# Kernel optimization log

Measured on AMD Instinct MI355X. Metric: run time of the kernel, lower is better.

The kernel has to match this reference:

```python
import jax, jax.numpy as jnp
import numpy as np

ALPHA = 1.702
LIMIT = 7.0

# Tiling: A*B*M = BD*S (total dispatched tokens)
A, B, E, M, H, I = 2, 8, 16, 128, 2048, 2048
_BD, _S = 2, 1024


def setup_inputs() -> dict:
    key = jax.random.key(0)
    ks = jax.random.split(key, 6)
    inv_h = 1.0 / np.sqrt(H)
    inv_i = 1.0 / np.sqrt(I)
    return {
        "dispatched": jax.random.normal(ks[0], (A, B, E, M, H), dtype=jnp.float32),
        "gate_up_proj": jax.random.normal(ks[1], (E, H, 2 * I), dtype=jnp.float32) * inv_h,
        "gate_up_proj_bias": jax.random.normal(ks[2], (E, 2 * I), dtype=jnp.float32) * 0.02,
        "down_proj": jax.random.normal(ks[3], (E, I, H), dtype=jnp.float32) * inv_i,
        "down_proj_bias": jax.random.normal(ks[4], (E, H), dtype=jnp.float32) * 0.02,
        "sparsity_remap": jax.random.randint(ks[5], (E, E), 0, E, dtype=jnp.int32),
        "BD": _BD,
        "S": _S,
    }


def _moe_activation_gpt_oss(gate_up_out):
    # interleaved gate/up: [g0,u0,g1,u1,...]
    gate = gate_up_out[..., ::2]
    up = gate_up_out[..., 1::2]
    gate = jnp.minimum(gate, LIMIT)
    up = jnp.clip(up, -LIMIT, LIMIT)
    glu = gate * jax.nn.sigmoid(gate * ALPHA)
    return (up + 1.0) * glu


def reference(dispatched, gate_up_proj, gate_up_proj_bias, down_proj,
              down_proj_bias, sparsity_remap, BD, S):
    # sparsity_remap is an opaque tile remap for tt.sparse_matmul; the dense
    # grouped matmul computes the same math (zero tiles contribute zeros).
    a, b, e, m, h = dispatched.shape
    inter = gate_up_proj.shape[-1] // 2
    # grouped gate_up GEMM: [A,B,E,M,H] @ [E,H,2I] -> [A,B,E,M,2I]
    gate_up_out = jnp.einsum('abemh,ehn->abemn', dispatched, gate_up_proj)
    gate_up_out = gate_up_out + gate_up_proj_bias[None, None, :, None, :]
    activated = _moe_activation_gpt_oss(gate_up_out)  # [A,B,E,M,I]
    activated = activated.reshape(a * b, e, m, inter)
    # grouped down GEMM: [AB,E,M,I] @ [E,I,H] -> [AB,E,M,H]
    down_out = jnp.einsum('xemi,eih->xemh', activated, down_proj)
    down_out = down_out + down_proj_bias[None, :, None, :]
    # untile: [AB,E,M,H] -> [AB,M,E,H] -> [BD,S,E,H]
    down_out = jnp.transpose(down_out, (0, 2, 1, 3))
    return down_out.reshape(BD, S, e, h)
```

## Files before the change

kernel.cpp:

```cpp
#include <hip/hip_runtime.h>
#include <stdint.h>

#define DEV __device__ __forceinline__

constexpr int E_ = 16, M_ = 128, H_ = 2048, I_ = 2048;
constexpr int X_ = 16;
constexpr int N1 = 2 * I_;
constexpr int ROWS = X_ * M_;

typedef short bfrag __attribute__((ext_vector_type(8)));
typedef float ffrag __attribute__((ext_vector_type(4)));
typedef unsigned short us8 __attribute__((ext_vector_type(8)));

DEV unsigned short f2bf(float f) {
    union { float f; unsigned u; } v; v.f = f;
    unsigned u = v.u;
    u += 0x7fffu + ((u >> 16) & 1u);
    return (unsigned short)(u >> 16);
}

DEV void gload16(const void* g, void* lds_wave_base) {
    __builtin_amdgcn_global_load_lds(
        (const __attribute__((address_space(1))) unsigned int*)g,
        (__attribute__((address_space(3))) unsigned int*)lds_wave_base,
        16, 0, 0);
}

DEV void block_bar() {
    asm volatile("" ::: "memory");
    __builtin_amdgcn_s_barrier();
    asm volatile("" ::: "memory");
}


__global__ __launch_bounds__(256) void convert_a(const float* __restrict__ in,
                                                 unsigned short* __restrict__ outb) {
    const int n4 = X_ * E_ * M_ * H_ / 4;
    int idx = blockIdx.x * 256 + threadIdx.x;
    int stride = gridDim.x * 256;
    for (int f = idx; f < n4; f += stride) {
        float4 v = ((const float4*)in)[f];
        ushort4 o;
        o.x = f2bf(v.x); o.y = f2bf(v.y); o.z = f2bf(v.z); o.w = f2bf(v.w);
        const int c = f & 511;
        const int row = f >> 9;
        const int m = row & 127, e = (row >> 7) & 15, x = row >> 11;
        ((ushort4*)outb)[((size_t)(e * ROWS + x * M_ + m) << 9) + c] = o;
    }
}

__global__ __launch_bounds__(256) void convert_b1(const float* __restrict__ gup,
                                                  unsigned short* __restrict__ b1t) {
    const int e = blockIdx.x, h0 = blockIdx.y * 64, n0 = blockIdx.z * 128;
    __shared__ float2 tile2[64][64];
    const float* src = gup + (size_t)e * H_ * N1;
    const int t = threadIdx.x;
#pragma unroll
    for (int i = 0; i < 8; ++i) {
        int idx = i * 1024 + t * 4;
        int r = idx >> 7, c = idx & 127;
        float4 v = *(const float4*)(src + (size_t)(h0 + r) * N1 + n0 + c);
        *(float4*)&tile2[r][c >> 1] = v;
    }
    __syncthreads();
    const int p = t >> 2;
    const int hh = (t & 3) * 16;
    us8 g0, g1, u0, u1;
#pragma unroll
    for (int k = 0; k < 8; ++k) {
        float2 a = tile2[hh + k][p];
        float2 b = tile2[hh + 8 + k][p];
        g0[k] = f2bf(a.x); u0[k] = f2bf(a.y);
        g1[k] = f2bf(b.x); u1[k] = f2bf(b.y);
    }
    unsigned short* dg = b1t + ((size_t)e * N1 + (n0 >> 1) + p) * H_ + h0 + hh;
    unsigned short* du = b1t + ((size_t)e * N1 + I_ + (n0 >> 1) + p) * H_ + h0 + hh;
    *(us8*)dg = g0; *(us8*)(dg + 8) = g1;
    *(us8*)du = u0; *(us8*)(du + 8) = u1;
}

__global__ __launch_bounds__(256) void convert_b2(const float* __restrict__ dwn,
                                                  unsigned short* __restrict__ b2t) {
    const int e = blockIdx.x, i0 = blockIdx.y * 64, h0 = blockIdx.z * 64;
    __shared__ float tile[64][65];
    const float* src = dwn + (size_t)e * I_ * H_;
    const int t = threadIdx.x;
#pragma unroll
    for (int it = 0; it < 4; ++it) {
        int idx = it * 1024 + t * 4;
        int r = idx >> 6, c = idx & 63;
        float4 v = *(const float4*)(src + (size_t)(i0 + r) * H_ + h0 + c);
        tile[r][c] = v.x; tile[r][c + 1] = v.y; tile[r][c + 2] = v.z; tile[r][c + 3] = v.w;
    }
    __syncthreads();
    const int hl = t >> 2, ii = (t & 3) * 16;
    us8 o0, o1;
#pragma unroll
    for (int k = 0; k < 8; ++k) {
        o0[k] = f2bf(tile[ii + k][hl]);
        o1[k] = f2bf(tile[ii + 8 + k][hl]);
    }
    unsigned short* d = b2t + ((size_t)e * H_ + h0 + hl) * I_ + i0 + ii;
    *(us8*)d = o0; *(us8*)(d + 8) = o1;
}

template <int MODE>
__global__ __launch_bounds__(512, 2) void gemm8p(
    const unsigned short* __restrict__ A,
    const unsigned short* __restrict__ B,
    const float* __restrict__ bias,
    void* __restrict__ outv)
{
    constexpr int LD = 2048;
    constexpr int NT = 2048 / 64;

    __shared__ unsigned short lds[2][2][256 * 64];

    const int t = threadIdx.x, wave = t >> 6, lane = t & 63;
    const int wr = wave >> 2, wc = wave & 3;

    int id = blockIdx.x;
    const int cpx = gridDim.x >> 3;
    id = (id & 7) * cpx + (id >> 3);
    int e, mt, bt;
    if (MODE == 0) { e = id >> 7; mt = (id >> 4) & 7; bt = id & 15; }
    else           { e = id >> 6; mt = (id >> 3) & 7; bt = id & 7; }

    const unsigned short* Aexp = A + ((size_t)e * ROWS + mt * 256) * LD;
    const unsigned short* Bexp = (MODE == 0)
        ? B + (size_t)e * N1 * LD
        : B + ((size_t)e * H_ + bt * 256) * LD;

    ffrag acc[8][4];
#pragma unroll
    for (int i = 0; i < 8; ++i)
#pragma unroll
        for (int j = 0; j < 4; ++j) acc[i][j] = ffrag{0.f, 0.f, 0.f, 0.f};

    const int rsub = lane >> 3;
    const int csw = ((lane & 7) ^ (lane >> 3)) * 8;

    auto stage = [&](int kt, int b) {
        const int k0 = kt * 64;
#pragma unroll
        for (int i = 0; i < 4; ++i) {
            const int Rb = (wave * 4 + i) * 8;
            const int r = Rb + rsub;
            gload16(Aexp + (size_t)r * LD + k0 + csw, (void*)&lds[b][0][Rb * 64]);
        }
#pragma unroll
        for (int i = 0; i < 4; ++i) {
            const int Rb = (wave * 4 + i) * 8;
            const int r = Rb + rsub;
            int grow;
            if (MODE == 0)
                grow = ((r >> 5) & 1) * I_ + bt * 128 + (r >> 6) * 32 + (r & 31);
            else
                grow = r;
            gload16(Bexp + (size_t)grow * LD + k0 + csw, (void*)&lds[b][1][Rb * 64]);
        }
    };

    stage(0, 0);

    const int l15 = lane & 15, lr16 = lane >> 4, sw = lane & 7;
    const int arow0 = wr * 128 + l15;
    const int brow0 = wc * 64 + l15;

#pragma unroll 2
    for (int kt = 0; kt < NT; ++kt) {
        const int cur = kt & 1;

        asm volatile("s_waitcnt vmcnt(0)" ::: "memory");
        __builtin_amdgcn_sched_barrier(0);
        block_bar();

        bfrag bB0[2][2], bB1[2][2];
        bfrag af[4][2];

#pragma unroll
        for (int nf = 0; nf < 2; ++nf)
#pragma unroll
            for (int ks = 0; ks < 2; ++ks)
                bB0[nf][ks] = *(const bfrag*)&lds[cur][1][(brow0 + nf * 16) * 64 + (((ks * 4 + lr16) ^ sw) * 8)];
#pragma unroll
        for (int mf = 0; mf < 4; ++mf)
#pragma unroll
            for (int ks = 0; ks < 2; ++ks)
                af[mf][ks] = *(const bfrag*)&lds[cur][0][(arow0 + mf * 16) * 64 + (((ks * 4 + lr16) ^ sw) * 8)];
        asm volatile("" ::: "memory");
#pragma unroll
        for (int nf = 0; nf < 2; ++nf)
#pragma unroll
            for (int ks = 0; ks < 2; ++ks)
                bB1[nf][ks] = *(const bfrag*)&lds[cur][1][(brow0 + 32 + nf * 16) * 64 + (((ks * 4 + lr16) ^ sw) * 8)];

        if (kt + 1 < NT) stage(kt + 1, cur ^ 1);

        asm volatile("s_waitcnt lgkmcnt(4)" ::: "memory");
        __builtin_amdgcn_sched_barrier(0);
        __builtin_amdgcn_s_setprio(1);
#pragma unroll
        for (int mf = 0; mf < 4; ++mf)
#pragma unroll
            for (int nf = 0; nf < 2; ++nf)
#pragma unroll
                for (int ks = 0; ks < 2; ++ks)
                    acc[mf][nf] = __builtin_amdgcn_mfma_f32_16x16x32_bf16(
                        af[mf][ks], bB0[nf][ks], acc[mf][nf], 0, 0, 0);
        __builtin_amdgcn_s_setprio(0);

        asm volatile("s_waitcnt lgkmcnt(0)" ::: "memory");
        __builtin_amdgcn_sched_barrier(0);
        __builtin_amdgcn_s_setprio(1);
#pragma unroll
        for (int mf = 0; mf < 4; ++mf)
#pragma unroll
            for (int nf = 0; nf < 2; ++nf)
#pragma unroll
                for (int ks = 0; ks < 2; ++ks)
                    acc[mf][2 + nf] = __builtin_amdgcn_mfma_f32_16x16x32_bf16(
                        af[mf][ks], bB1[nf][ks], acc[mf][2 + nf], 0, 0, 0);
        __builtin_amdgcn_s_setprio(0);

        bfrag ag[4][2];
#pragma unroll
        for (int mf = 0; mf < 4; ++mf)
#pragma unroll
            for (int ks = 0; ks < 2; ++ks)
                ag[mf][ks] = *(const bfrag*)&lds[cur][0][(arow0 + 64 + mf * 16) * 64 + (((ks * 4 + lr16) ^ sw) * 8)];

        asm volatile("s_waitcnt lgkmcnt(4)" ::: "memory");
        __builtin_amdgcn_sched_barrier(0);
        __builtin_amdgcn_s_setprio(1);
#pragma unroll
        for (int mf = 0; mf < 2; ++mf)
#pragma unroll
            for (int nf = 0; nf < 2; ++nf)
#pragma unroll
                for (int ks = 0; ks < 2; ++ks)
                    acc[4 + mf][2 + nf] = __builtin_amdgcn_mfma_f32_16x16x32_bf16(
                        ag[mf][ks], bB1[nf][ks], acc[4 + mf][2 + nf], 0, 0, 0);
        __builtin_amdgcn_s_setprio(0);

        asm volatile("s_waitcnt lgkmcnt(0)" ::: "memory");
        __builtin_amdgcn_sched_barrier(0);
        __builtin_amdgcn_s_setprio(1);
#pragma unroll
        for (int mf = 2; mf < 4; ++mf)
#pragma unroll
            for (int nf = 0; nf < 2; ++nf)
#pragma unroll
                for (int ks = 0; ks < 2; ++ks)
                    acc[4 + mf][2 + nf] = __builtin_amdgcn_mfma_f32_16x16x32_bf16(
                        ag[mf][ks], bB1[nf][ks], acc[4 + mf][2 + nf], 0, 0, 0);
#pragma unroll
        for (int mf = 0; mf < 4; ++mf)
#pragma unroll
            for (int nf = 0; nf < 2; ++nf)
#pragma unroll
                for (int ks = 0; ks < 2; ++ks)
                    acc[4 + mf][nf] = __builtin_amdgcn_mfma_f32_16x16x32_bf16(
                        ag[mf][ks], bB0[nf][ks], acc[4 + mf][nf], 0, 0, 0);
        __builtin_amdgcn_s_setprio(0);
    }

    const int rb = mt * 256 + wr * 128 + lr16 * 4;
    if (MODE == 0) {
        unsigned short* act = (unsigned short*)outv + (size_t)e * ROWS * I_;
#pragma unroll
        for (int nf = 0; nf < 2; ++nf) {
            const int jj = bt * 128 + wc * 32 + nf * 16 + l15;
            const float gb = bias[(size_t)e * N1 + 2 * jj];
            const float ub = bias[(size_t)e * N1 + 2 * jj + 1];
#pragma unroll
            for (int mf = 0; mf < 8; ++mf)
#pragma unroll
                for (int r = 0; r < 4; ++r) {
                    float g = acc[mf][nf][r] + gb;
                    float u = acc[mf][2 + nf][r] + ub;
                    g = fminf(g, 7.0f);
                    u = fminf(fmaxf(u, -7.0f), 7.0f);
                    const float glu = g / (1.0f + __expf(-1.702f * g));
                    const float av = (u + 1.0f) * glu;
                    act[(size_t)(rb + mf * 16 + r) * I_ + jj] = f2bf(av);
                }
        }
    } else {
        float* out = (float*)outv;
#pragma unroll
        for (int nf = 0; nf < 4; ++nf) {
            const int h = bt * 256 + wc * 64 + nf * 16 + l15;
            const float bb = bias[(size_t)e * H_ + h];
#pragma unroll
            for (int mf = 0; mf < 8; ++mf)
#pragma unroll
                for (int r = 0; r < 4; ++r) {
                    const int row = rb + mf * 16 + r;
                    out[((size_t)row * E_ + e) * H_ + h] = acc[mf][nf][r] + bb;
                }
        }
    }
}


extern "C" void kernel_launch(void* const* d_in, const int* in_sizes, int n_in,
                              void* d_out, int out_size, void* d_ws, size_t ws_size,
                              hipStream_t stream) {
    const float* disp  = (const float*)d_in[0];
    const float* gup   = (const float*)d_in[1];
    const float* gub   = (const float*)d_in[2];
    const float* down  = (const float*)d_in[3];
    const float* dbias = (const float*)d_in[4];
    float* out = (float*)d_out;

    const size_t NEED = (size_t)512 << 20;
    if (ws_size < NEED) {
        hipMemsetAsync(d_out, 0, (size_t)out_size * sizeof(float), stream);
        return;
    }
    unsigned short* a_bf = (unsigned short*)d_ws;
    unsigned short* b1t  = (unsigned short*)((char*)d_ws + ((size_t)128 << 20));
    unsigned short* b2t  = b1t;
    unsigned short* actb = (unsigned short*)((char*)d_ws + ((size_t)384 << 20));

    convert_a<<<4096, 256, 0, stream>>>(disp, a_bf);
    convert_b1<<<dim3(E_, H_ / 64, N1 / 128), 256, 0, stream>>>(gup, b1t);
    gemm8p<0><<<2048, 512, 0, stream>>>(a_bf, b1t, gub, actb);
    convert_b2<<<dim3(E_, I_ / 64, H_ / 64), 256, 0, stream>>>(down, b2t);
    gemm8p<1><<<1024, 512, 0, stream>>>(actb, b2t, dbias, out);
}
```

Measured before the change: 1.102 ms.

## Switch GEMM inner loop from 16x16x32 to 32x32x16 bf16 MFMA tiles

Replaces the 16x16x32 MFMA fragments with 32x32x16 MFMA instructions, so each wave holds a 4x2 grid of 32x32 accumulator tiles instead of an 8x4 grid of 16x16 tiles. The LDS fragment loads, swizzle indexing, K-step schedule and epilogue row mapping are all rewritten to match the 32x32 output layout. The aim is fewer MFMA issues and fewer LDS fragment reads per unit of work, since the larger tile reuses each operand more. It changes register pressure and the LDS access pattern, and the epilogue writes follow a different lane-to-row mapping.

```diff
diff --git a/kernel.cpp b/kernel.cpp
--- a/kernel.cpp
+++ b/kernel.cpp
@@ -9,7 +9,7 @@
 constexpr int ROWS = X_ * M_;
 
 typedef short bfrag __attribute__((ext_vector_type(8)));
-typedef float ffrag __attribute__((ext_vector_type(4)));
+typedef float f32x16 __attribute__((ext_vector_type(16)));
 typedef unsigned short us8 __attribute__((ext_vector_type(8)));
 
 DEV unsigned short f2bf(float f) {
@@ -131,11 +131,13 @@
         ? B + (size_t)e * N1 * LD
         : B + ((size_t)e * H_ + bt * 256) * LD;
 
-    ffrag acc[8][4];
-#pragma unroll
-    for (int i = 0; i < 8; ++i)
-#pragma unroll
-        for (int j = 0; j < 4; ++j) acc[i][j] = ffrag{0.f, 0.f, 0.f, 0.f};
+    f32x16 acc[4][2];
+#pragma unroll
+    for (int i = 0; i < 4; ++i)
+#pragma unroll
+        for (int j = 0; j < 2; ++j)
+#pragma unroll
+            for (int r = 0; r < 16; ++r) acc[i][j][r] = 0.f;
 
     const int rsub = lane >> 3;
     const int csw = ((lane & 7) ^ (lane >> 3)) * 8;
@@ -163,9 +165,12 @@
 
     stage(0, 0);
 
-    const int l15 = lane & 15, lr16 = lane >> 4, sw = lane & 7;
-    const int arow0 = wr * 128 + l15;
-    const int brow0 = wc * 64 + l15;
+    const int l31 = lane & 31, lr32 = lane >> 5, l7 = lane & 7;
+    const int arow0 = wr * 128 + l31;
+    const int brow0 = wc * 64 + l31;
+
+#define AIDX(MT_, KS_) ((arow0 + (MT_) * 32) * 64 + ((((KS_) * 2 + lr32) ^ l7) * 8))
+#define BIDX(NT_, KS_) ((brow0 + (NT_) * 32) * 64 + ((((KS_) * 2 + lr32) ^ l7) * 8))
 
 #pragma unroll 2
     for (int kt = 0; kt < NT; ++kt) {
@@ -175,130 +180,118 @@
         __builtin_amdgcn_sched_barrier(0);
         block_bar();
 
-        bfrag bB0[2][2], bB1[2][2];
-        bfrag af[4][2];
-
-#pragma unroll
-        for (int nf = 0; nf < 2; ++nf)
+        bfrag bK[2][2], aK0[4], aK1[4];
+
+#pragma unroll
+        for (int nt = 0; nt < 2; ++nt)
 #pragma unroll
             for (int ks = 0; ks < 2; ++ks)
-                bB0[nf][ks] = *(const bfrag*)&lds[cur][1][(brow0 + nf * 16) * 64 + (((ks * 4 + lr16) ^ sw) * 8)];
-#pragma unroll
-        for (int mf = 0; mf < 4; ++mf)
+                bK[nt][ks] = *(const bfrag*)&lds[cur][1][BIDX(nt, ks)];
+#pragma unroll
+        for (int mt_i = 0; mt_i < 4; ++mt_i)
+            aK0[mt_i] = *(const bfrag*)&lds[cur][0][AIDX(mt_i, 0)];
+        asm volatile("" ::: "memory");
+#pragma unroll
+        for (int mt_i = 0; mt_i < 4; ++mt_i)
+            aK1[mt_i] = *(const bfrag*)&lds[cur][0][AIDX(mt_i, 1)];
+
+        if (kt + 1 < NT) stage(kt + 1, cur ^ 1);
+
+        asm volatile("s_waitcnt lgkmcnt(4)" ::: "memory");
+        __builtin_amdgcn_sched_barrier(0);
+        __builtin_amdgcn_s_setprio(1);
+#pragma unroll
+        for (int mt_i = 0; mt_i < 4; ++mt_i)
+#pragma unroll
+            for (int nt = 0; nt < 2; ++nt)
+                acc[mt_i][nt] = __builtin_amdgcn_mfma_f32_32x32x16_bf16(
+                    aK0[mt_i], bK[nt][0], acc[mt_i][nt], 0, 0, 0);
+        __builtin_amdgcn_s_setprio(0);
+
+        asm volatile("s_waitcnt lgkmcnt(0)" ::: "memory");
+        __builtin_amdgcn_sched_barrier(0);
+        __builtin_amdgcn_s_setprio(1);
+#pragma unroll
+        for (int mt_i = 0; mt_i < 4; ++mt_i)
+#pragma unroll
+            for (int nt = 0; nt < 2; ++nt)
+                acc[mt_i][nt] = __builtin_amdgcn_mfma_f32_32x32x16_bf16(
+                    aK1[mt_i], bK[nt][1], acc[mt_i][nt], 0, 0, 0);
+        __builtin_amdgcn_s_setprio(0);
+
+        bfrag bL[2][2], aK2[4], aK3[4];
+#pragma unroll
+        for (int nt = 0; nt < 2; ++nt)
 #pragma unroll
             for (int ks = 0; ks < 2; ++ks)
-                af[mf][ks] = *(const bfrag*)&lds[cur][0][(arow0 + mf * 16) * 64 + (((ks * 4 + lr16) ^ sw) * 8)];
+                bL[nt][ks] = *(const bfrag*)&lds[cur][1][BIDX(nt, 2 + ks)];
+#pragma unroll
+        for (int mt_i = 0; mt_i < 4; ++mt_i)
+            aK2[mt_i] = *(const bfrag*)&lds[cur][0][AIDX(mt_i, 2)];
         asm volatile("" ::: "memory");
 #pragma unroll
-        for (int nf = 0; nf < 2; ++nf)
-#pragma unroll
-            for (int ks = 0; ks < 2; ++ks)
-                bB1[nf][ks] = *(const bfrag*)&lds[cur][1][(brow0 + 32 + nf * 16) * 64 + (((ks * 4 + lr16) ^ sw) * 8)];
-
-        if (kt + 1 < NT) stage(kt + 1, cur ^ 1);
+        for (int mt_i = 0; mt_i < 4; ++mt_i)
+            aK3[mt_i] = *(const bfrag*)&lds[cur][0][AIDX(mt_i, 3)];
 
         asm volatile("s_waitcnt lgkmcnt(4)" ::: "memory");
         __builtin_amdgcn_sched_barrier(0);
         __builtin_amdgcn_s_setprio(1);
 #pragma unroll
-        for (int mf = 0; mf < 4; ++mf)
-#pragma unroll
-            for (int nf = 0; nf < 2; ++nf)
-#pragma unroll
-                for (int ks = 0; ks < 2; ++ks)
-                    acc[mf][nf] = __builtin_amdgcn_mfma_f32_16x16x32_bf16(
-                        af[mf][ks], bB0[nf][ks], acc[mf][nf], 0, 0, 0);
+        for (int mt_i = 0; mt_i < 4; ++mt_i)
+#pragma unroll
+            for (int nt = 0; nt < 2; ++nt)
+                acc[mt_i][nt] = __builtin_amdgcn_mfma_f32_32x32x16_bf16(
+                    aK2[mt_i], bL[nt][0], acc[mt_i][nt], 0, 0, 0);
         __builtin_amdgcn_s_setprio(0);
 
         asm volatile("s_waitcnt lgkmcnt(0)" ::: "memory");
         __builtin_amdgcn_sched_barrier(0);
         __builtin_amdgcn_s_setprio(1);
 #pragma unroll
-        for (int mf = 0; mf < 4; ++mf)
-#pragma unroll
-            for (int nf = 0; nf < 2; ++nf)
-#pragma unroll
-                for (int ks = 0; ks < 2; ++ks)
-                    acc[mf][2 + nf] = __builtin_amdgcn_mfma_f32_16x16x32_bf16(
-                        af[mf][ks], bB1[nf][ks], acc[mf][2 + nf], 0, 0, 0);
+        for (int mt_i = 0; mt_i < 4; ++mt_i)
+#pragma unroll
+            for (int nt = 0; nt < 2; ++nt)
+                acc[mt_i][nt] = __builtin_amdgcn_mfma_f32_32x32x16_bf16(
+                    aK3[mt_i], bL[nt][1], acc[mt_i][nt], 0, 0, 0);
         __builtin_amdgcn_s_setprio(0);
-
-        bfrag ag[4][2];
-#pragma unroll
-        for (int mf = 0; mf < 4; ++mf)
-#pragma unroll
-            for (int ks = 0; ks < 2; ++ks)
-                ag[mf][ks] = *(const bfrag*)&lds[cur][0][(arow0 + 64 + mf * 16) * 64 + (((ks * 4 + lr16) ^ sw) * 8)];
-
-        asm volatile("s_waitcnt lgkmcnt(4)" ::: "memory");
-        __builtin_amdgcn_sched_barrier(0);
-        __builtin_amdgcn_s_setprio(1);
-#pragma unroll
-        for (int mf = 0; mf < 2; ++mf)
-#pragma unroll
-            for (int nf = 0; nf < 2; ++nf)
-#pragma unroll
-                for (int ks = 0; ks < 2; ++ks)
-                    acc[4 + mf][2 + nf] = __builtin_amdgcn_mfma_f32_16x16x32_bf16(
-                        ag[mf][ks], bB1[nf][ks], acc[4 + mf][2 + nf], 0, 0, 0);
-        __builtin_amdgcn_s_setprio(0);
-
-        asm volatile("s_waitcnt lgkmcnt(0)" ::: "memory");
-        __builtin_amdgcn_sched_barrier(0);
-        __builtin_amdgcn_s_setprio(1);
-#pragma unroll
-        for (int mf = 2; mf < 4; ++mf)
-#pragma unroll
-            for (int nf = 0; nf < 2; ++nf)
-#pragma unroll
-                for (int ks = 0; ks < 2; ++ks)
-                    acc[4 + mf][2 + nf] = __builtin_amdgcn_mfma_f32_16x16x32_bf16(
-                        ag[mf][ks], bB1[nf][ks], acc[4 + mf][2 + nf], 0, 0, 0);
-#pragma unroll
-        for (int mf = 0; mf < 4; ++mf)
-#pragma unroll
-            for (int nf = 0; nf < 2; ++nf)
-#pragma unroll
-                for (int ks = 0; ks < 2; ++ks)
-                    acc[4 + mf][nf] = __builtin_amdgcn_mfma_f32_16x16x32_bf16(
-                        ag[mf][ks], bB0[nf][ks], acc[4 + mf][nf], 0, 0, 0);
-        __builtin_amdgcn_s_setprio(0);
-    }
-
-    const int rb = mt * 256 + wr * 128 + lr16 * 4;
+    }
+#undef AIDX
+#undef BIDX
+
+    const int rb = mt * 256 + wr * 128;
     if (MODE == 0) {
         unsigned short* act = (unsigned short*)outv + (size_t)e * ROWS * I_;
-#pragma unroll
-        for (int nf = 0; nf < 2; ++nf) {
-            const int jj = bt * 128 + wc * 32 + nf * 16 + l15;
-            const float gb = bias[(size_t)e * N1 + 2 * jj];
-            const float ub = bias[(size_t)e * N1 + 2 * jj + 1];
-#pragma unroll
-            for (int mf = 0; mf < 8; ++mf)
-#pragma unroll
-                for (int r = 0; r < 4; ++r) {
-                    float g = acc[mf][nf][r] + gb;
-                    float u = acc[mf][2 + nf][r] + ub;
-                    g = fminf(g, 7.0f);
-                    u = fminf(fmaxf(u, -7.0f), 7.0f);
-                    const float glu = g / (1.0f + __expf(-1.702f * g));
-                    const float av = (u + 1.0f) * glu;
-                    act[(size_t)(rb + mf * 16 + r) * I_ + jj] = f2bf(av);
-                }
+        const int jj = bt * 128 + wc * 32 + l31;
+        const float gb = bias[(size_t)e * N1 + 2 * jj];
+        const float ub = bias[(size_t)e * N1 + 2 * jj + 1];
+#pragma unroll
+        for (int mt_i = 0; mt_i < 4; ++mt_i) {
+#pragma unroll
+            for (int reg = 0; reg < 16; ++reg) {
+                const int row = rb + mt_i * 32 + (reg & 3) + 8 * (reg >> 2) + 4 * lr32;
+                float g = acc[mt_i][0][reg] + gb;
+                float u = acc[mt_i][1][reg] + ub;
+                g = fminf(g, 7.0f);
+                u = fminf(fmaxf(u, -7.0f), 7.0f);
+                const float glu = g / (1.0f + __expf(-1.702f * g));
+                const float av = (u + 1.0f) * glu;
+                act[(size_t)row * I_ + jj] = f2bf(av);
+            }
         }
     } else {
         float* out = (float*)outv;
 #pragma unroll
-        for (int nf = 0; nf < 4; ++nf) {
-            const int h = bt * 256 + wc * 64 + nf * 16 + l15;
+        for (int nt = 0; nt < 2; ++nt) {
+            const int h = bt * 256 + wc * 64 + nt * 32 + l31;
             const float bb = bias[(size_t)e * H_ + h];
 #pragma unroll
-            for (int mf = 0; mf < 8; ++mf)
-#pragma unroll
-                for (int r = 0; r < 4; ++r) {
-                    const int row = rb + mf * 16 + r;
-                    out[((size_t)row * E_ + e) * H_ + h] = acc[mf][nf][r] + bb;
+            for (int mt_i = 0; mt_i < 4; ++mt_i) {
+#pragma unroll
+                for (int reg = 0; reg < 16; ++reg) {
+                    const int row = rb + mt_i * 32 + (reg & 3) + 8 * (reg >> 2) + 4 * lr32;
+                    out[((size_t)row * E_ + e) * H_ + h] = acc[mt_i][nt][reg] + bb;
                 }
+            }
         }
     }
 }
```

Result: slower. 1.163 ms (+5.5%).

## Split A/B staging into halves and interleave with MFMA phases across barriers

Applied to the files above, without the earlier changes.

Splits the global-to-LDS staging into half-tile A and B loads spread across the four MFMA phases. The B tile is now prefetched two k-steps ahead into the buffer being consumed, while A is prefetched one step ahead, so memory loads overlap compute at finer granularity. The price is many extra block barriers per k-iteration and tighter vmcnt bookkeeping, and the change to in-place B buffer reuse adds correctness and ordering risk.

```diff
diff --git a/kernel.cpp b/kernel.cpp
--- a/kernel.cpp
+++ b/kernel.cpp
@@ -140,17 +140,20 @@
     const int rsub = lane >> 3;
     const int csw = ((lane & 7) ^ (lane >> 3)) * 8;
 
-    auto stage = [&](int kt, int b) {
+    auto stageA = [&](int kt, int b, int half) {
         const int k0 = kt * 64;
 #pragma unroll
-        for (int i = 0; i < 4; ++i) {
-            const int Rb = (wave * 4 + i) * 8;
+        for (int i = 0; i < 2; ++i) {
+            const int Rb = half * 128 + (wave * 2 + i) * 8;
             const int r = Rb + rsub;
             gload16(Aexp + (size_t)r * LD + k0 + csw, (void*)&lds[b][0][Rb * 64]);
         }
-#pragma unroll
-        for (int i = 0; i < 4; ++i) {
-            const int Rb = (wave * 4 + i) * 8;
+    };
+    auto stageB = [&](int kt, int b, int half) {
+        const int k0 = kt * 64;
+#pragma unroll
+        for (int i = 0; i < 2; ++i) {
+            const int Rb = half * 128 + (wave * 2 + i) * 8;
             const int r = Rb + rsub;
             int grow;
             if (MODE == 0)
@@ -161,43 +164,36 @@
         }
     };
 
-    stage(0, 0);
+    stageA(0, 0, 0); stageA(0, 0, 1);
+    stageB(0, 0, 0); stageB(0, 0, 1);
+    stageB(1, 1, 0); stageB(1, 1, 1);
+    asm volatile("s_waitcnt vmcnt(4)" ::: "memory");
+    __builtin_amdgcn_sched_barrier(0);
+    block_bar();
 
     const int l15 = lane & 15, lr16 = lane >> 4, sw = lane & 7;
     const int arow0 = wr * 128 + l15;
     const int brow0 = wc * 64 + l15;
 
-#pragma unroll 2
     for (int kt = 0; kt < NT; ++kt) {
         const int cur = kt & 1;
-
-        asm volatile("s_waitcnt vmcnt(0)" ::: "memory");
-        __builtin_amdgcn_sched_barrier(0);
-        block_bar();
-
-        bfrag bB0[2][2], bB1[2][2];
-        bfrag af[4][2];
+        bfrag bB0[2][2], bB1[2][2], af[4][2], ag[4][2];
 
 #pragma unroll
         for (int nf = 0; nf < 2; ++nf)
 #pragma unroll
             for (int ks = 0; ks < 2; ++ks)
                 bB0[nf][ks] = *(const bfrag*)&lds[cur][1][(brow0 + nf * 16) * 64 + (((ks * 4 + lr16) ^ sw) * 8)];
+        asm volatile("" ::: "memory");
 #pragma unroll
         for (int mf = 0; mf < 4; ++mf)
 #pragma unroll
             for (int ks = 0; ks < 2; ++ks)
                 af[mf][ks] = *(const bfrag*)&lds[cur][0][(arow0 + mf * 16) * 64 + (((ks * 4 + lr16) ^ sw) * 8)];
-        asm volatile("" ::: "memory");
-#pragma unroll
-        for (int nf = 0; nf < 2; ++nf)
-#pragma unroll
-            for (int ks = 0; ks < 2; ++ks)
-                bB1[nf][ks] = *(const bfrag*)&lds[cur][1][(brow0 + 32 + nf * 16) * 64 + (((ks * 4 + lr16) ^ sw) * 8)];
-
-        if (kt + 1 < NT) stage(kt + 1, cur ^ 1);
-
-        asm volatile("s_waitcnt lgkmcnt(4)" ::: "memory");
+        if (kt + 1 < NT) stageA(kt + 1, cur ^ 1, 0);
+        asm volatile("s_waitcnt lgkmcnt(8)" ::: "memory");
+        block_bar();
+        asm volatile("s_waitcnt lgkmcnt(0)" ::: "memory");
         __builtin_amdgcn_sched_barrier(0);
         __builtin_amdgcn_s_setprio(1);
 #pragma unroll
@@ -209,7 +205,15 @@
                     acc[mf][nf] = __builtin_amdgcn_mfma_f32_16x16x32_bf16(
                         af[mf][ks], bB0[nf][ks], acc[mf][nf], 0, 0, 0);
         __builtin_amdgcn_s_setprio(0);
-
+        block_bar();
+
+#pragma unroll
+        for (int nf = 0; nf < 2; ++nf)
+#pragma unroll
+            for (int ks = 0; ks < 2; ++ks)
+                bB1[nf][ks] = *(const bfrag*)&lds[cur][1][(brow0 + 32 + nf * 16) * 64 + (((ks * 4 + lr16) ^ sw) * 8)];
+        if (kt + 1 < NT) stageA(kt + 1, cur ^ 1, 1);
+        block_bar();
         asm volatile("s_waitcnt lgkmcnt(0)" ::: "memory");
         __builtin_amdgcn_sched_barrier(0);
         __builtin_amdgcn_s_setprio(1);
@@ -222,19 +226,20 @@
                     acc[mf][2 + nf] = __builtin_amdgcn_mfma_f32_16x16x32_bf16(
                         af[mf][ks], bB1[nf][ks], acc[mf][2 + nf], 0, 0, 0);
         __builtin_amdgcn_s_setprio(0);
-
-        bfrag ag[4][2];
+        block_bar();
+
 #pragma unroll
         for (int mf = 0; mf < 4; ++mf)
 #pragma unroll
             for (int ks = 0; ks < 2; ++ks)
                 ag[mf][ks] = *(const bfrag*)&lds[cur][0][(arow0 + 64 + mf * 16) * 64 + (((ks * 4 + lr16) ^ sw) * 8)];
-
-        asm volatile("s_waitcnt lgkmcnt(4)" ::: "memory");
+        if (kt + 2 < NT) stageB(kt + 2, cur, 0);
+        block_bar();
+        asm volatile("s_waitcnt lgkmcnt(0)" ::: "memory");
         __builtin_amdgcn_sched_barrier(0);
         __builtin_amdgcn_s_setprio(1);
 #pragma unroll
-        for (int mf = 0; mf < 2; ++mf)
+        for (int mf = 0; mf < 4; ++mf)
 #pragma unroll
             for (int nf = 0; nf < 2; ++nf)
 #pragma unroll
@@ -242,18 +247,11 @@
                     acc[4 + mf][2 + nf] = __builtin_amdgcn_mfma_f32_16x16x32_bf16(
                         ag[mf][ks], bB1[nf][ks], acc[4 + mf][2 + nf], 0, 0, 0);
         __builtin_amdgcn_s_setprio(0);
-
-        asm volatile("s_waitcnt lgkmcnt(0)" ::: "memory");
-        __builtin_amdgcn_sched_barrier(0);
+        block_bar();
+
+        if (kt + 2 < NT) stageB(kt + 2, cur, 1);
+        block_bar();
         __builtin_amdgcn_s_setprio(1);
-#pragma unroll
-        for (int mf = 2; mf < 4; ++mf)
-#pragma unroll
-            for (int nf = 0; nf < 2; ++nf)
-#pragma unroll
-                for (int ks = 0; ks < 2; ++ks)
-                    acc[4 + mf][2 + nf] = __builtin_amdgcn_mfma_f32_16x16x32_bf16(
-                        ag[mf][ks], bB1[nf][ks], acc[4 + mf][2 + nf], 0, 0, 0);
 #pragma unroll
         for (int mf = 0; mf < 4; ++mf)
 #pragma unroll
@@ -263,6 +261,10 @@
                     acc[4 + mf][nf] = __builtin_amdgcn_mfma_f32_16x16x32_bf16(
                         ag[mf][ks], bB0[nf][ks], acc[4 + mf][nf], 0, 0, 0);
         __builtin_amdgcn_s_setprio(0);
+        if (kt + 2 < NT)      { asm volatile("s_waitcnt vmcnt(4)" ::: "memory"); }
+        else if (kt + 1 < NT) { asm volatile("s_waitcnt vmcnt(0)" ::: "memory"); }
+        __builtin_amdgcn_sched_barrier(0);
+        if (kt + 1 < NT) block_bar();
     }
 
     const int rb = mt * 256 + wr * 128 + lr16 * 4;
```

Result: no change. 1.112 ms (+0.8%).
